# Kernel tuning notes

Hardware: AMD Instinct MI355X
Metric: run time of the kernel (lower is better)

## Reference

```python
import jax, jax.numpy as jnp
import numpy as np

N_NODES = 50000
N_EDGES = 1600000
CHANNELS = 128
EXPANSION = 50
CUTOFF = 5.0
LOG2 = 0.6931471805599453


def shifted_softplus(x):
    return jax.nn.softplus(x) - LOG2


def gaussian_smearing(r, cutoff=CUTOFF, n=EXPANSION):
    # centers evenly spaced in [0, cutoff]; width set by spacing
    centers = jnp.linspace(0.0, cutoff, n, dtype=r.dtype)
    delta = centers[1] - centers[0]
    coef = 1.0 / (2.0 * delta * delta)
    d = r[:, None] - centers[None, :]          # [E, n]
    return jnp.exp(-coef * d * d)


def setup_inputs() -> dict:
    key = jax.random.key(0)
    ks = jax.random.split(key, 12)
    C, F = CHANNELS, EXPANSION

    def lin(k, fan_in, shape):
        bound = 1.0 / np.sqrt(fan_in)
        return jax.random.uniform(k, shape, jnp.float32, -bound, bound)

    return {
        "features": jax.random.normal(ks[0], (N_NODES, C), jnp.float32),
        "edge_distances": jax.random.uniform(ks[1], (N_EDGES,), jnp.float32) * CUTOFF,
        "W_lin": lin(ks[2], C, (C, C)),
        "Wf1": lin(ks[3], F, (F, C)), "bf1": lin(ks[4], F, (C,)),
        "Wf2": lin(ks[5], C, (C, C)), "bf2": lin(ks[6], C, (C,)),
        "Wm1": lin(ks[7], C, (C, C)), "bm1": lin(ks[8], C, (C,)),
        "Wm2": lin(ks[9], C, (C, C)), "bm2": lin(ks[10], C, (C,)),
        "senders": jax.random.randint(ks[11], (N_EDGES,), 0, N_NODES, jnp.int32),
        "receivers": jax.random.randint(jax.random.fold_in(key, 99), (N_EDGES,), 0, N_NODES, jnp.int32),
    }


def reference(features, edge_distances, W_lin, Wf1, bf1, Wf2, bf2,
              Wm1, bm1, Wm2, bm2, senders, receivers):
    # 1. linear transform of node features (no bias)
    h = features @ W_lin.T                                   # [N, C]
    # 2. learnable radial filter F(r_ij): Gaussian basis -> MLP
    basis = gaussian_smearing(edge_distances)                # [E, F]
    ef = shifted_softplus(basis @ Wf1 + bf1) @ Wf2 + bf2     # [E, C]
    # 3. gather neighbour features, elementwise multiply, scatter-sum
    messages = h[senders] * ef                               # [E, C]
    agg = jax.ops.segment_sum(messages, receivers, num_segments=N_NODES)  # [N, C]
    # 4. output MLP
    return shifted_softplus(agg @ Wm1 + bm1) @ Wm2 + bm2
```

## Files before the change

kernel.cpp:

```cpp
#include <hip/hip_runtime.h>
#include <hip/hip_bf16.h>
#include <math.h>

#define N_NODES 50000
#define N_EDGES 1600000
#define CH 128
#define NF 50
#define NR 8192
#define NB 1563
#define BUCKET_NODES 32
#define CAP 1280
#define RECS_PT 5
#define PASSA_CHUNK 2048
#define NBLK_SCAT 782
#define NBLK_TB   128
#define NBLK_DH   782

constexpr float DELTA  = 5.0f / 49.0f;
constexpr float COEF   = 1.0f / (2.0f * DELTA * DELTA);
constexpr float LOG2_  = 0.6931471805599453f;
constexpr float RSCALE = (float)(NR - 1) / 5.0f;

typedef short  bf16x8 __attribute__((ext_vector_type(8)));
typedef float  f32x4  __attribute__((ext_vector_type(4)));
typedef unsigned short ushort_t;
typedef unsigned long long u64;

__device__ __forceinline__ float ssp(float x) {
    return fmaxf(x, 0.0f) + __logf(1.0f + __expf(-fabsf(x))) - LOG2_;
}
__device__ __forceinline__ ushort_t f2bf(float x) {
    __hip_bfloat16 b = __float2bfloat16(x);
    return *reinterpret_cast<ushort_t*>(&b);
}
__device__ __forceinline__ float bf2f(ushort_t u) {
    return __uint_as_float(((unsigned)u) << 16);
}
__device__ __forceinline__ float4 f4zero() { return make_float4(0.f, 0.f, 0.f, 0.f); }

__global__ __launch_bounds__(256) void k1_prep(const float* __restrict__ Wlin,
                                               const float* __restrict__ Wm1,
                                               const float* __restrict__ Wm2,
                                               const float* __restrict__ Wf1,
                                               const float* __restrict__ Wf2,
                                               ushort_t* __restrict__ wlhi,
                                               ushort_t* __restrict__ wllo,
                                               ushort_t* __restrict__ wm1hi,
                                               ushort_t* __restrict__ wm1lo,
                                               ushort_t* __restrict__ wm2hi,
                                               ushort_t* __restrict__ wm2lo,
                                               ushort_t* __restrict__ wf1t,
                                               ushort_t* __restrict__ wf2hi,
                                               ushort_t* __restrict__ wf2lo,
                                               int* __restrict__ bcnt) {
    const int tid = threadIdx.x;
    if (blockIdx.x == 64) {
        for (int i = tid; i < NB; i += 256) bcnt[i] = 0;
        return;
    }
    int idx = blockIdx.x * 256 + tid;
    int n = idx >> 7, k = idx & 127;
    {   float w = Wlin[(size_t)n * CH + k];
        ushort_t hi = f2bf(w); wlhi[n * CH + k] = hi; wllo[n * CH + k] = f2bf(w - bf2f(hi)); }
    {   float w = Wm1[(size_t)k * CH + n];
        ushort_t hi = f2bf(w); wm1hi[n * CH + k] = hi; wm1lo[n * CH + k] = f2bf(w - bf2f(hi)); }
    {   float w = Wm2[(size_t)k * CH + n];
        ushort_t hi = f2bf(w); wm2hi[n * CH + k] = hi; wm2lo[n * CH + k] = f2bf(w - bf2f(hi)); }
    if (k < 64) wf1t[n * 64 + k] = (k < NF) ? f2bf(Wf1[k * CH + n]) : (ushort_t)0;
    {   float w = Wf2[(size_t)k * CH + n];
        ushort_t hi = f2bf(w); wf2hi[n * CH + k] = hi; wf2lo[n * CH + k] = f2bf(w - bf2f(hi)); }
}

__device__ void scatter_body(char* smem, int blk,
                             const int* __restrict__ recv,
                             const int* __restrict__ send,
                             const float* __restrict__ dist,
                             int* __restrict__ bcnt,
                             u64* __restrict__ brec) {
    int* bcur   = (int*)smem;
    int* bbaseL = bcur + NB;
    const int tid = threadIdx.x;
    for (int i = tid; i < NB; i += 256) bcur[i] = 0;
    __syncthreads();
    const int e0 = blk * PASSA_CHUNK;
    const bool full = (e0 + PASSA_CHUNK <= N_EDGES);
    int r8[8];
    if (full) {
#pragma unroll
        for (int i = 0; i < 8; i++) r8[i] = recv[e0 + tid + i * 256];
#pragma unroll
        for (int i = 0; i < 8; i++) atomicAdd(&bcur[r8[i] / BUCKET_NODES], 1);
    } else {
#pragma unroll
        for (int i = 0; i < 8; i++) {
            int e = e0 + tid + i * 256;
            r8[i] = (e < N_EDGES) ? recv[e] : -1;
            if (r8[i] >= 0) atomicAdd(&bcur[r8[i] / BUCKET_NODES], 1);
        }
    }
    __syncthreads();
    for (int i = tid; i < NB; i += 256) {
        int c = bcur[i];
        bbaseL[i] = c ? atomicAdd(&bcnt[i], c) : 0;
        bcur[i] = 0;
    }
    __syncthreads();
    if (full) {
        int s8[8]; float d8[8];
#pragma unroll
        for (int i = 0; i < 8; i++) {
            int e = e0 + tid + i * 256;
            s8[i] = send[e];
            d8[i] = dist[e];
        }
#pragma unroll
        for (int i = 0; i < 8; i++) {
            int b = r8[i] / BUCKET_NODES;
            int rank = bbaseL[b] + atomicAdd(&bcur[b], 1);
            if (rank < CAP) {
                int ti = __float2int_rn(fminf(d8[i] * RSCALE, (float)(NR - 1)));
                u64 rec = (u64)(unsigned)(s8[i] | (r8[i] << 16)) | ((u64)ti << 32);
                brec[(size_t)b * CAP + rank] = rec;
            }
        }
    } else {
#pragma unroll
        for (int i = 0; i < 8; i++) {
            int e = e0 + tid + i * 256;
            if (e < N_EDGES) {
                int r = r8[i];
                int b = r / BUCKET_NODES;
                int rank = bbaseL[b] + atomicAdd(&bcur[b], 1);
                if (rank < CAP) {
                    int ti = __float2int_rn(fminf(dist[e] * RSCALE, (float)(NR - 1)));
                    u64 rec = (u64)(unsigned)(send[e] | (r << 16)) | ((u64)ti << 32);
                    brec[(size_t)b * CAP + rank] = rec;
                }
            }
        }
    }
}

__device__ void table_body(char* smem, int blk,
                           const float* __restrict__ bf1,
                           const float* __restrict__ bf2,
                           const ushort_t* __restrict__ wf1t,
                           const ushort_t* __restrict__ wf2hi,
                           const ushort_t* __restrict__ wf2lo,
                           ushort_t* __restrict__ tabn) {
    ushort_t (*basis)[72] = (ushort_t (*)[72])smem;
    ushort_t (*t1s)[136]  = (ushort_t (*)[136])(smem + 64 * 72 * 2);
    const int tid = threadIdx.x;
    const int g0  = blk * 64;

    for (int i = tid; i < 64 * 64; i += 256) {
        int e = i >> 6, k = i & 63;
        float val = 0.f;
        if (k < NF) {
            float r = (float)(g0 + e) * (5.0f / (float)(NR - 1));
            float d = r - (float)k * DELTA;
            val = __expf(-COEF * d * d);
        }
        basis[e][k] = f2bf(val);
    }
    __syncthreads();

    const int lane = tid & 63;
    const int wv   = tid >> 6;
    const int row  = lane & 15;
    const int quad = lane >> 4;
    const int c0   = (2 * wv) * 16 + row;
    const int c1   = c0 + 16;

    f32x4 acc[2][4];
#pragma unroll
    for (int j = 0; j < 2; j++)
#pragma unroll
        for (int rt = 0; rt < 4; rt++) acc[j][rt] = (f32x4){0.f, 0.f, 0.f, 0.f};

#pragma unroll
    for (int kb = 0; kb < 64; kb += 32) {
        bf16x8 B0 = *(const bf16x8*)&wf1t[c0 * 64 + kb + quad * 8];
        bf16x8 B1 = *(const bf16x8*)&wf1t[c1 * 64 + kb + quad * 8];
#pragma unroll
        for (int rt = 0; rt < 4; rt++) {
            bf16x8 A = *(const bf16x8*)&basis[rt * 16 + row][kb + quad * 8];
            acc[0][rt] = __builtin_amdgcn_mfma_f32_16x16x32_bf16(A, B0, acc[0][rt], 0, 0, 0);
            acc[1][rt] = __builtin_amdgcn_mfma_f32_16x16x32_bf16(A, B1, acc[1][rt], 0, 0, 0);
        }
    }
    {
        float b1v[2] = { bf1[c0], bf1[c1] };
#pragma unroll
        for (int j = 0; j < 2; j++) {
            int c = j ? c1 : c0;
#pragma unroll
            for (int rt = 0; rt < 4; rt++)
#pragma unroll
                for (int rg = 0; rg < 4; rg++) {
                    int e = rt * 16 + quad * 4 + rg;
                    t1s[e][c] = f2bf(ssp(acc[j][rt][rg] + b1v[j]));
                }
        }
    }
    __syncthreads();

#pragma unroll
    for (int j = 0; j < 2; j++)
#pragma unroll
        for (int rt = 0; rt < 4; rt++) acc[j][rt] = (f32x4){0.f, 0.f, 0.f, 0.f};

#pragma unroll
    for (int kb = 0; kb < 128; kb += 32) {
        bf16x8 B0h = *(const bf16x8*)&wf2hi[c0 * CH + kb + quad * 8];
        bf16x8 B0l = *(const bf16x8*)&wf2lo[c0 * CH + kb + quad * 8];
        bf16x8 B1h = *(const bf16x8*)&wf2hi[c1 * CH + kb + quad * 8];
        bf16x8 B1l = *(const bf16x8*)&wf2lo[c1 * CH + kb + quad * 8];
#pragma unroll
        for (int rt = 0; rt < 4; rt++) {
            bf16x8 A = *(const bf16x8*)&t1s[rt * 16 + row][kb + quad * 8];
            acc[0][rt] = __builtin_amdgcn_mfma_f32_16x16x32_bf16(A, B0l, acc[0][rt], 0, 0, 0);
            acc[0][rt] = __builtin_amdgcn_mfma_f32_16x16x32_bf16(A, B0h, acc[0][rt], 0, 0, 0);
            acc[1][rt] = __builtin_amdgcn_mfma_f32_16x16x32_bf16(A, B1l, acc[1][rt], 0, 0, 0);
            acc[1][rt] = __builtin_amdgcn_mfma_f32_16x16x32_bf16(A, B1h, acc[1][rt], 0, 0, 0);
        }
    }
    {
        float b2v[2] = { bf2[c0], bf2[c1] };
#pragma unroll
        for (int j = 0; j < 2; j++) {
            int c = j ? c1 : c0;
#pragma unroll
            for (int rt = 0; rt < 4; rt++)
#pragma unroll
                for (int rg = 0; rg < 4; rg++) {
                    int g = g0 + rt * 16 + quad * 4 + rg;
                    tabn[(size_t)g * CH + c] = f2bf(acc[j][rt][rg] + b2v[j]);
                }
        }
    }
}

__device__ void dense_h_body(char* smem, int blk,
                             const float* __restrict__ X,
                             const ushort_t* __restrict__ Bhi,
                             const ushort_t* __restrict__ Blo,
                             ushort_t* __restrict__ Y) {
    ushort_t (*xs)[136] = (ushort_t (*)[136])smem;
    const int tid  = threadIdx.x;
    const int row0 = blk * 64;

#pragma unroll
    for (int i = 0; i < 8; i++) {
        int idx = tid + i * 256;
        int r   = idx >> 5;
        int c4  = (idx & 31) * 4;
        float4 v = (row0 + r < N_NODES) ? *(const float4*)&X[(size_t)(row0 + r) * CH + c4]
                                        : f4zero();
        ushort4 s;
        s.x = f2bf(v.x); s.y = f2bf(v.y); s.z = f2bf(v.z); s.w = f2bf(v.w);
        *(ushort4*)&xs[r][c4] = s;
    }
    __syncthreads();

    const int lane = tid & 63;
    const int wv   = tid >> 6;
    const int row  = lane & 15;
    const int quad = lane >> 4;
    const int c0   = (2 * wv) * 16 + row;
    const int c1   = c0 + 16;

    f32x4 acc[2][4];
#pragma unroll
    for (int j = 0; j < 2; j++)
#pragma unroll
        for (int rt = 0; rt < 4; rt++) acc[j][rt] = (f32x4){0.f, 0.f, 0.f, 0.f};

#pragma unroll
    for (int kb = 0; kb < 128; kb += 32) {
        bf16x8 B0h = *(const bf16x8*)&Bhi[(size_t)c0 * CH + kb + quad * 8];
        bf16x8 B0l = *(const bf16x8*)&Blo[(size_t)c0 * CH + kb + quad * 8];
        bf16x8 B1h = *(const bf16x8*)&Bhi[(size_t)c1 * CH + kb + quad * 8];
        bf16x8 B1l = *(const bf16x8*)&Blo[(size_t)c1 * CH + kb + quad * 8];
#pragma unroll
        for (int rt = 0; rt < 4; rt++) {
            bf16x8 A = *(const bf16x8*)&xs[rt * 16 + row][kb + quad * 8];
            acc[0][rt] = __builtin_amdgcn_mfma_f32_16x16x32_bf16(A, B0l, acc[0][rt], 0, 0, 0);
            acc[0][rt] = __builtin_amdgcn_mfma_f32_16x16x32_bf16(A, B0h, acc[0][rt], 0, 0, 0);
            acc[1][rt] = __builtin_amdgcn_mfma_f32_16x16x32_bf16(A, B1l, acc[1][rt], 0, 0, 0);
            acc[1][rt] = __builtin_amdgcn_mfma_f32_16x16x32_bf16(A, B1h, acc[1][rt], 0, 0, 0);
        }
    }

#pragma unroll
    for (int j = 0; j < 2; j++) {
        int c = j ? c1 : c0;
#pragma unroll
        for (int rt = 0; rt < 4; rt++)
#pragma unroll
            for (int rg = 0; rg < 4; rg++) {
                int r = row0 + rt * 16 + quad * 4 + rg;
                if (r < N_NODES) Y[(size_t)r * CH + c] = f2bf(acc[j][rt][rg]);
            }
    }
}

__global__ __launch_bounds__(256) void k2_mega(const int* __restrict__ recv,
                                               const int* __restrict__ send,
                                               const float* __restrict__ dist,
                                               int* __restrict__ bcnt,
                                               u64* __restrict__ brec,
                                               const float* __restrict__ bf1,
                                               const float* __restrict__ bf2,
                                               const ushort_t* __restrict__ wf1t,
                                               const ushort_t* __restrict__ wf2hi,
                                               const ushort_t* __restrict__ wf2lo,
                                               ushort_t* __restrict__ tabn,
                                               const float* __restrict__ X,
                                               const ushort_t* __restrict__ wlhi,
                                               const ushort_t* __restrict__ wllo,
                                               ushort_t* __restrict__ h) {
    __shared__ __align__(16) char smem[64 * 72 * 2 + 64 * 136 * 2];
    const int blk = blockIdx.x;
    if (blk < NBLK_SCAT) {
        scatter_body(smem, blk, recv, send, dist, bcnt, brec);
    } else if (blk < NBLK_SCAT + NBLK_TB) {
        table_body(smem, blk - NBLK_SCAT, bf1, bf2, wf1t, wf2hi, wf2lo, tabn);
    } else {
        dense_h_body(smem, blk - NBLK_SCAT - NBLK_TB, X, wlhi, wllo, h);
    }
}

__global__ __launch_bounds__(256) void sort_gather_mlp(const int* __restrict__ bcnt,
                                                       const u64* __restrict__ brec,
                                                       const ushort_t* __restrict__ h,
                                                       const ushort_t* __restrict__ tabn,
                                                       const ushort_t* __restrict__ B1hi,
                                                       const ushort_t* __restrict__ B1lo,
                                                       const float* __restrict__ bm1,
                                                       const ushort_t* __restrict__ B2hi,
                                                       const ushort_t* __restrict__ B2lo,
                                                       const float* __restrict__ bm2,
                                                       float* __restrict__ OUT) {
    __shared__ int shist[BUCKET_NODES];
    __shared__ int sbeg[BUCKET_NODES];
    __shared__ int sexc[BUCKET_NODES];
    __shared__ unsigned sout[CAP];
    __shared__ __align__(16) ushort_t at[32][136];
    const int b = blockIdx.x, tid = threadIdx.x;
    const int nbase = b * BUCKET_NODES;
    const int nn = min(BUCKET_NODES, N_NODES - nbase);
    if (nn <= 0) return;
    const int m = min(bcnt[b], CAP);
    const u64* my = brec + (size_t)b * CAP;

    if (tid < BUCKET_NODES) shist[tid] = 0;
    for (int i = tid; i < 32 * 17; i += 256) {
        bf16x8 z = (bf16x8){0, 0, 0, 0, 0, 0, 0, 0};
        *(bf16x8*)&at[i / 17][(i % 17) * 8] = z;
    }
    __syncthreads();

    unsigned pw0 = 0, pw1 = 0, pw2 = 0, pw3 = 0, pw4 = 0;
    int lc0 = -1, lc1 = -1, lc2 = -1, lc3 = -1, lc4 = -1;
    {
        int i;
        i = tid;           if (i < m) { u64 rec = my[i]; lc0 = (int)((rec >> 16) & 0xFFFF) - nbase; pw0 = (unsigned)(rec & 0xFFFF) | ((unsigned)((rec >> 32) & 0x3FFF) << 16); }
        i = tid + 256;     if (i < m) { u64 rec = my[i]; lc1 = (int)((rec >> 16) & 0xFFFF) - nbase; pw1 = (unsigned)(rec & 0xFFFF) | ((unsigned)((rec >> 32) & 0x3FFF) << 16); }
        i = tid + 512;     if (i < m) { u64 rec = my[i]; lc2 = (int)((rec >> 16) & 0xFFFF) - nbase; pw2 = (unsigned)(rec & 0xFFFF) | ((unsigned)((rec >> 32) & 0x3FFF) << 16); }
        i = tid + 768;     if (i < m) { u64 rec = my[i]; lc3 = (int)((rec >> 16) & 0xFFFF) - nbase; pw3 = (unsigned)(rec & 0xFFFF) | ((unsigned)((rec >> 32) & 0x3FFF) << 16); }
        i = tid + 1024;    if (i < m) { u64 rec = my[i]; lc4 = (int)((rec >> 16) & 0xFFFF) - nbase; pw4 = (unsigned)(rec & 0xFFFF) | ((unsigned)((rec >> 32) & 0x3FFF) << 16); }
        if (lc0 >= 0) atomicAdd(&shist[lc0], 1);
        if (lc1 >= 0) atomicAdd(&shist[lc1], 1);
        if (lc2 >= 0) atomicAdd(&shist[lc2], 1);
        if (lc3 >= 0) atomicAdd(&shist[lc3], 1);
        if (lc4 >= 0) atomicAdd(&shist[lc4], 1);
    }
    __syncthreads();
    if (tid == 0) {
        int acc = 0;
#pragma unroll
        for (int l = 0; l < BUCKET_NODES; l++) {
            sexc[l] = acc; sbeg[l] = acc; acc += shist[l];
        }
    }
    __syncthreads();
    {
        if (lc0 >= 0) { int rank = atomicAdd(&sexc[lc0], 1); sout[rank] = pw0; }
        if (lc1 >= 0) { int rank = atomicAdd(&sexc[lc1], 1); sout[rank] = pw1; }
        if (lc2 >= 0) { int rank = atomicAdd(&sexc[lc2], 1); sout[rank] = pw2; }
        if (lc3 >= 0) { int rank = atomicAdd(&sexc[lc3], 1); sout[rank] = pw3; }
        if (lc4 >= 0) { int rank = atomicAdd(&sexc[lc4], 1); sout[rank] = pw4; }
    }
    __syncthreads();

    {
        const int g  = tid >> 4;
        const int c8 = (tid & 15) * 8;
        for (int l = g; l < nn; l += 16) {
            const int beg = sbeg[l], end = sbeg[l] + shist[l];
            float acc[8];
#pragma unroll
            for (int j = 0; j < 8; j++) acc[j] = 0.f;

            int e = beg;
            for (; e + 8 <= end; e += 8) {
                unsigned v[8];
#pragma unroll
                for (int u = 0; u < 8; u++) v[u] = sout[e + u];
                bf16x8 hu[8], tn[8];
#pragma unroll
                for (int u = 0; u < 8; u++) {
                    int s  = (int)(v[u] & 0xFFFF);
                    int ti = (int)(v[u] >> 16);
                    hu[u] = *(const bf16x8*)&h[(size_t)s * CH + c8];
                    tn[u] = *(const bf16x8*)&tabn[(size_t)ti * CH + c8];
                }
#pragma unroll
                for (int u = 0; u < 8; u++)
#pragma unroll
                    for (int j = 0; j < 8; j++)
                        acc[j] = fmaf(bf2f((ushort_t)hu[u][j]), bf2f((ushort_t)tn[u][j]), acc[j]);
            }
            for (; e + 4 <= end; e += 4) {
                unsigned v[4];
#pragma unroll
                for (int u = 0; u < 4; u++) v[u] = sout[e + u];
                bf16x8 hu[4], tn[4];
#pragma unroll
                for (int u = 0; u < 4; u++) {
                    int s  = (int)(v[u] & 0xFFFF);
                    int ti = (int)(v[u] >> 16);
                    hu[u] = *(const bf16x8*)&h[(size_t)s * CH + c8];
                    tn[u] = *(const bf16x8*)&tabn[(size_t)ti * CH + c8];
                }
#pragma unroll
                for (int u = 0; u < 4; u++)
#pragma unroll
                    for (int j = 0; j < 8; j++)
                        acc[j] = fmaf(bf2f((ushort_t)hu[u][j]), bf2f((ushort_t)tn[u][j]), acc[j]);
            }
            for (; e < end; e++) {
                unsigned v = sout[e];
                int s  = (int)(v & 0xFFFF);
                int ti = (int)(v >> 16);
                bf16x8 hu = *(const bf16x8*)&h[(size_t)s * CH + c8];
                bf16x8 tn = *(const bf16x8*)&tabn[(size_t)ti * CH + c8];
#pragma unroll
                for (int j = 0; j < 8; j++)
                    acc[j] = fmaf(bf2f((ushort_t)hu[j]), bf2f((ushort_t)tn[j]), acc[j]);
            }

            bf16x8 o;
#pragma unroll
            for (int j = 0; j < 8; j++) o[j] = (short)f2bf(acc[j]);
            *(bf16x8*)&at[l][c8] = o;
        }
    }
    __syncthreads();

    const int lane = tid & 63;
    const int wv   = tid >> 6;
    const int row  = lane & 15;
    const int quad = lane >> 4;
    const int c0   = (2 * wv) * 16 + row;
    const int c1   = c0 + 16;

    f32x4 acc[2][2];
#pragma unroll
    for (int j = 0; j < 2; j++)
#pragma unroll
        for (int rt = 0; rt < 2; rt++) acc[j][rt] = (f32x4){0.f, 0.f, 0.f, 0.f};

#pragma unroll
    for (int kb = 0; kb < 128; kb += 32) {
        bf16x8 B0h = *(const bf16x8*)&B1hi[(size_t)c0 * CH + kb + quad * 8];
        bf16x8 B0l = *(const bf16x8*)&B1lo[(size_t)c0 * CH + kb + quad * 8];
        bf16x8 B1h_ = *(const bf16x8*)&B1hi[(size_t)c1 * CH + kb + quad * 8];
        bf16x8 B1l_ = *(const bf16x8*)&B1lo[(size_t)c1 * CH + kb + quad * 8];
#pragma unroll
        for (int rt = 0; rt < 2; rt++) {
            bf16x8 A = *(const bf16x8*)&at[rt * 16 + row][kb + quad * 8];
            acc[0][rt] = __builtin_amdgcn_mfma_f32_16x16x32_bf16(A, B0l, acc[0][rt], 0, 0, 0);
            acc[0][rt] = __builtin_amdgcn_mfma_f32_16x16x32_bf16(A, B0h, acc[0][rt], 0, 0, 0);
            acc[1][rt] = __builtin_amdgcn_mfma_f32_16x16x32_bf16(A, B1l_, acc[1][rt], 0, 0, 0);
            acc[1][rt] = __builtin_amdgcn_mfma_f32_16x16x32_bf16(A, B1h_, acc[1][rt], 0, 0, 0);
        }
    }
    __syncthreads();
    {
        float bv[2] = { bm1[c0], bm1[c1] };
#pragma unroll
        for (int j = 0; j < 2; j++) {
            int c = j ? c1 : c0;
#pragma unroll
            for (int rt = 0; rt < 2; rt++)
#pragma unroll
                for (int rg = 0; rg < 4; rg++)
                    at[rt * 16 + quad * 4 + rg][c] = f2bf(ssp(acc[j][rt][rg] + bv[j]));
        }
    }
    __syncthreads();

#pragma unroll
    for (int j = 0; j < 2; j++)
#pragma unroll
        for (int rt = 0; rt < 2; rt++) acc[j][rt] = (f32x4){0.f, 0.f, 0.f, 0.f};

#pragma unroll
    for (int kb = 0; kb < 128; kb += 32) {
        bf16x8 B0h = *(const bf16x8*)&B2hi[(size_t)c0 * CH + kb + quad * 8];
        bf16x8 B0l = *(const bf16x8*)&B2lo[(size_t)c0 * CH + kb + quad * 8];
        bf16x8 B1h_ = *(const bf16x8*)&B2hi[(size_t)c1 * CH + kb + quad * 8];
        bf16x8 B1l_ = *(const bf16x8*)&B2lo[(size_t)c1 * CH + kb + quad * 8];
#pragma unroll
        for (int rt = 0; rt < 2; rt++) {
            bf16x8 A = *(const bf16x8*)&at[rt * 16 + row][kb + quad * 8];
            acc[0][rt] = __builtin_amdgcn_mfma_f32_16x16x32_bf16(A, B0l, acc[0][rt], 0, 0, 0);
            acc[0][rt] = __builtin_amdgcn_mfma_f32_16x16x32_bf16(A, B0h, acc[0][rt], 0, 0, 0);
            acc[1][rt] = __builtin_amdgcn_mfma_f32_16x16x32_bf16(A, B1l_, acc[1][rt], 0, 0, 0);
            acc[1][rt] = __builtin_amdgcn_mfma_f32_16x16x32_bf16(A, B1h_, acc[1][rt], 0, 0, 0);
        }
    }
    {
        float bv[2] = { bm2[c0], bm2[c1] };
#pragma unroll
        for (int j = 0; j < 2; j++) {
            int c = j ? c1 : c0;
#pragma unroll
            for (int rt = 0; rt < 2; rt++)
#pragma unroll
                for (int rg = 0; rg < 4; rg++) {
                    int r = rt * 16 + quad * 4 + rg;
                    if (r < nn) OUT[(size_t)(nbase + r) * CH + c] = acc[j][rt][rg] + bv[j];
                }
        }
    }
}

extern "C" void kernel_launch(void* const* d_in, const int* in_sizes, int n_in,
                              void* d_out, int out_size, void* d_ws, size_t ws_size,
                              hipStream_t stream) {
    const float* features = (const float*)d_in[0];
    const float* dist     = (const float*)d_in[1];
    const float* W_lin    = (const float*)d_in[2];
    const float* Wf1      = (const float*)d_in[3];
    const float* bf1      = (const float*)d_in[4];
    const float* Wf2      = (const float*)d_in[5];
    const float* bf2      = (const float*)d_in[6];
    const float* Wm1      = (const float*)d_in[7];
    const float* bm1      = (const float*)d_in[8];
    const float* Wm2      = (const float*)d_in[9];
    const float* bm2      = (const float*)d_in[10];
    const int* senders    = (const int*)d_in[11];
    const int* receivers  = (const int*)d_in[12];
    float* out = (float*)d_out;

    u64* brec       = (u64*)d_ws;
    ushort_t* h     = (ushort_t*)(brec + (size_t)NB * CAP);
    ushort_t* tabn  = h + (size_t)N_NODES * CH;
    int* bcnt       = (int*)(tabn + (size_t)NR * CH);
    ushort_t* wlhi  = (ushort_t*)(bcnt + NB);
    ushort_t* wllo  = wlhi  + CH * CH;
    ushort_t* wm1hi = wllo  + CH * CH;
    ushort_t* wm1lo = wm1hi + CH * CH;
    ushort_t* wm2hi = wm1lo + CH * CH;
    ushort_t* wm2lo = wm2hi + CH * CH;
    ushort_t* wf1t  = wm2lo + CH * CH;
    ushort_t* wf2hi = wf1t  + CH * 64;
    ushort_t* wf2lo = wf2hi + CH * CH;

    k1_prep<<<65, 256, 0, stream>>>(W_lin, Wm1, Wm2, Wf1, Wf2,
                                    wlhi, wllo, wm1hi, wm1lo, wm2hi, wm2lo,
                                    wf1t, wf2hi, wf2lo, bcnt);

    k2_mega<<<NBLK_SCAT + NBLK_TB + NBLK_DH, 256, 0, stream>>>(
        receivers, senders, dist, bcnt, brec,
        bf1, bf2, wf1t, wf2hi, wf2lo, tabn,
        features, wlhi, wllo, h);

    sort_gather_mlp<<<NB, 256, 0, stream>>>(bcnt, brec, h, tabn,
                                            wm1hi, wm1lo, bm1,
                                            wm2hi, wm2lo, bm2, out);
}
```

Baseline: 255.7 us.

## Balance per-node gather work by degree-sorted pairing and enlarge scatter chunks

```diff
diff --git a/kernel.cpp b/kernel.cpp
--- a/kernel.cpp
+++ b/kernel.cpp
@@ -10,9 +10,8 @@
 #define NB 1563
 #define BUCKET_NODES 32
 #define CAP 1280
-#define RECS_PT 5
-#define PASSA_CHUNK 2048
-#define NBLK_SCAT 782
+#define PASSA_CHUNK 4096
+#define NBLK_SCAT 391
 #define NBLK_TB   128
 #define NBLK_DH   782
 
@@ -83,20 +82,10 @@
     for (int i = tid; i < NB; i += 256) bcur[i] = 0;
     __syncthreads();
     const int e0 = blk * PASSA_CHUNK;
-    const bool full = (e0 + PASSA_CHUNK <= N_EDGES);
-    int r8[8];
-    if (full) {
-#pragma unroll
-        for (int i = 0; i < 8; i++) r8[i] = recv[e0 + tid + i * 256];
-#pragma unroll
-        for (int i = 0; i < 8; i++) atomicAdd(&bcur[r8[i] / BUCKET_NODES], 1);
-    } else {
-#pragma unroll
-        for (int i = 0; i < 8; i++) {
-            int e = e0 + tid + i * 256;
-            r8[i] = (e < N_EDGES) ? recv[e] : -1;
-            if (r8[i] >= 0) atomicAdd(&bcur[r8[i] / BUCKET_NODES], 1);
-        }
+#pragma unroll
+    for (int i = 0; i < 16; i++) {
+        int e = e0 + tid + i * 256;
+        if (e < N_EDGES) atomicAdd(&bcur[recv[e] / BUCKET_NODES], 1);
     }
     __syncthreads();
     for (int i = tid; i < NB; i += 256) {
@@ -105,37 +94,18 @@
         bcur[i] = 0;
     }
     __syncthreads();
-    if (full) {
-        int s8[8]; float d8[8];
-#pragma unroll
-        for (int i = 0; i < 8; i++) {
-            int e = e0 + tid + i * 256;
-            s8[i] = send[e];
-            d8[i] = dist[e];
-        }
-#pragma unroll
-        for (int i = 0; i < 8; i++) {
-            int b = r8[i] / BUCKET_NODES;
+#pragma unroll
+    for (int i = 0; i < 16; i++) {
+        int e = e0 + tid + i * 256;
+        if (e < N_EDGES) {
+            int r = recv[e];
+            int b = r / BUCKET_NODES;
             int rank = bbaseL[b] + atomicAdd(&bcur[b], 1);
             if (rank < CAP) {
-                int ti = __float2int_rn(fminf(d8[i] * RSCALE, (float)(NR - 1)));
-                u64 rec = (u64)(unsigned)(s8[i] | (r8[i] << 16)) | ((u64)ti << 32);
+                float x = fminf(dist[e] * RSCALE, (float)(NR - 1));
+                int ti = __float2int_rn(x);
+                u64 rec = (u64)(unsigned)(send[e] | (r << 16)) | ((u64)ti << 32);
                 brec[(size_t)b * CAP + rank] = rec;
-            }
-        }
-    } else {
-#pragma unroll
-        for (int i = 0; i < 8; i++) {
-            int e = e0 + tid + i * 256;
-            if (e < N_EDGES) {
-                int r = r8[i];
-                int b = r / BUCKET_NODES;
-                int rank = bbaseL[b] + atomicAdd(&bcur[b], 1);
-                if (rank < CAP) {
-                    int ti = __float2int_rn(fminf(dist[e] * RSCALE, (float)(NR - 1)));
-                    u64 rec = (u64)(unsigned)(send[e] | (r << 16)) | ((u64)ti << 32);
-                    brec[(size_t)b * CAP + rank] = rec;
-                }
             }
         }
     }
@@ -345,6 +315,7 @@
     __shared__ int shist[BUCKET_NODES];
     __shared__ int sbeg[BUCKET_NODES];
     __shared__ int sexc[BUCKET_NODES];
+    __shared__ int perm[BUCKET_NODES];
     __shared__ unsigned sout[CAP];
     __shared__ __align__(16) ushort_t at[32][136];
     const int b = blockIdx.x, tid = threadIdx.x;
@@ -385,6 +356,16 @@
         }
     }
     __syncthreads();
+    if (tid < BUCKET_NODES) {
+        int c = shist[tid];
+        int rank = 0;
+#pragma unroll
+        for (int j = 0; j < BUCKET_NODES; j++) {
+            int cj = shist[j];
+            rank += (cj > c) || (cj == c && j < tid);
+        }
+        perm[rank] = tid;
+    }
     {
         if (lc0 >= 0) { int rank = atomicAdd(&sexc[lc0], 1); sout[rank] = pw0; }
         if (lc1 >= 0) { int rank = atomicAdd(&sexc[lc1], 1); sout[rank] = pw1; }
@@ -397,7 +378,10 @@
     {
         const int g  = tid >> 4;
         const int c8 = (tid & 15) * 8;
-        for (int l = g; l < nn; l += 16) {
+#pragma unroll
+        for (int t = 0; t < 2; t++) {
+            const int l = perm[t ? (BUCKET_NODES - 1 - g) : g];
+            if (l >= nn) continue;
             const int beg = sbeg[l], end = sbeg[l] + shist[l];
             float acc[8];
 #pragma unroll
```

Result: no change. 253.8 us, median of 2 (-0.8%).
